# Kernel optimization log

Measured on AMD Instinct MI355X. Metric: run time of the kernel, lower is better.

## Reference

```python
import jax, jax.numpy as jnp
import numpy as np

B, NJ, COL = 16384, 14, 14
R = 4  # scipy gaussian_filter(sigma=1, truncate=4) -> radius int(4*1+0.5)=4


def _gauss_kernel(dtype):
    x = np.arange(-R, R + 1, dtype=np.float64)
    k = np.exp(-0.5 * x * x)
    k /= k.sum()
    return jnp.asarray(k, dtype)


def _gaussian_filter2d(x):
    # x: [B, Nj, COL, COL]; scipy mode='reflect' == jnp.pad mode='symmetric'
    k = _gauss_kernel(x.dtype)
    xp = jnp.pad(x, ((0, 0), (0, 0), (R, R), (R, R)), mode='symmetric')
    n = x.shape[0] * x.shape[1]
    xp = xp.reshape(n, 1, COL + 2 * R, COL + 2 * R)
    y = jax.lax.conv_general_dilated(xp, k.reshape(1, 1, 2 * R + 1, 1), (1, 1), 'VALID')
    y = jax.lax.conv_general_dilated(y, k.reshape(1, 1, 1, 2 * R + 1), (1, 1), 'VALID')
    return y.reshape(x.shape)


def setup_inputs() -> dict:
    key = jax.random.key(0)
    k1, k2, k3, k4, k5 = jax.random.split(key, 5)
    h = jax.random.uniform(k1, (B, NJ, COL, COL), jnp.float32)
    os_ = jax.random.normal(k2, (B, 2 * NJ, COL, COL), jnp.float32)
    op = jax.random.uniform(k3, (B, NJ, 3), jnp.float32)
    t = jax.random.uniform(k4, (B, NJ, 2), jnp.float32)
    vis = jax.random.randint(k5, (B, NJ, 1), 0, 2).astype(jnp.float32)
    v = jnp.concatenate([vis, vis], axis=-1)  # visibility duplicated, as assumed by v.sum()/2
    return {"os_": os_, "h": h, "op": op, "t": t, "v": v}


def reference(os_, h, op, t, v):
    scale = 1.0 / COL
    grid = jnp.arange(COL)

    # --- argmax decode of predicted heatmaps ---
    hf = h.reshape(-1, NJ, COL * COL)
    idx = jnp.argmax(hf, axis=-1)                 # [B, Nj]
    yC = idx // COL                               # integer division (old-torch LongTensor /)
    xC = idx - yC * COL
    hmax = jnp.max(hf, axis=-1)                   # h value at argmax
    osf = os_.reshape(-1, 2 * NJ, COL * COL)
    osx = jnp.take_along_axis(osf[:, :NJ], idx[..., None], axis=-1)[..., 0]
    osy = jnp.take_along_axis(osf[:, NJ:], idx[..., None], axis=-1)[..., 0]
    cond = hmax > 0.5
    x0 = jnp.where(cond, (osx + xC.astype(h.dtype)) * scale, 0.0)
    x1 = jnp.where(cond, (osy + yC.astype(h.dtype)) * scale, 0.0)
    x = jnp.stack([x0, x1], axis=-1)              # [B, Nj, 2]

    # --- gaussian splat of target coords into tt (only for visible joints) ---
    ti = t * COL
    xi = jnp.clip(jnp.trunc(ti[..., 0]).astype(jnp.int32), 0, COL - 1)
    yi = jnp.clip(jnp.trunc(ti[..., 1]).astype(jnp.int32), 0, COL - 1)
    onehot = ((grid[None, None, :, None] == yi[..., None, None]) &
              (grid[None, None, None, :] == xi[..., None, None])).astype(h.dtype)
    g = _gaussian_filter2d(onehot)
    mn = g.min(axis=(-2, -1), keepdims=True)
    mx = g.max(axis=(-2, -1), keepdims=True)
    gn = (g - mn) / (mx - mn)                     # min_max normalization
    vis = jnp.trunc(v[..., 0]).astype(jnp.int32) == 1  # int(v[i,j,0]) == 1
    tt = jnp.where(vis[..., None, None], gn, 0.0)

    # --- d1: heatmap MSE; for invisible joints only ROW 0 of diff is zeroed (faithful to source) ---
    diff1 = h - tt
    row0_mask = (~vis)[..., None, None] & (grid == 0)[None, None, :, None]
    diff1 = jnp.where(row0_mask, 0.0, diff1)
    N = v.sum() / 2
    d1 = jnp.sum(diff1 * diff1) / N

    # --- d2: decoded-coordinate MSE, visibility-masked ---
    diff2 = (x - t) * v
    d2 = jnp.sum(diff2 * diff2) / N

    return d1 + d2
```

## Files before the change

### kernel.cpp

```cpp
#include <hip/hip_runtime.h>
#include <math.h>

#define NB     16384
#define NJOINT 14
#define NCOL   14
#define NPIX   196
#define NTASKS (NB * NJOINT)
#define RAD    4

#define BLOCK1 256
#define GRID1  (NTASKS / BLOCK1)

typedef float f4 __attribute__((ext_vector_type(4)));

__global__ __launch_bounds__(BLOCK1) void mse2_main(
    const float* __restrict__ osp,
    const float* __restrict__ h,
    const float* __restrict__ t,
    const float* __restrict__ v,
    double* __restrict__ partials)
{
    __shared__ float tbl[NPIX];
    __shared__ float rmax[NCOL];
    __shared__ double sd[BLOCK1], sn[BLOCK1];

    const int tid = threadIdx.x;

    if (tid < NPIX) {
        double kd[2 * RAD + 1];
        double ks = 0.0;
        #pragma unroll
        for (int d = 0; d <= 2 * RAD; ++d) {
            double xx = (double)(d - RAD);
            kd[d] = exp(-0.5 * xx * xx);
            ks += kd[d];
        }
        const int p = tid / NCOL, o = tid % NCOL;
        float s = 0.f;
        #pragma unroll
        for (int d = 0; d <= 2 * RAD; ++d) {
            int i = o + d;
            int m = (i < RAD) ? (RAD - 1 - i)
                  : (i < RAD + NCOL) ? (i - RAD)
                  : (2 * (RAD + NCOL) - 1 - i - RAD);
            if (m == p) s += (float)(kd[d] / ks);
        }
        tbl[p * NCOL + o] = s;
    }
    __syncthreads();
    if (tid < NCOL) {
        float mxv = tbl[tid * NCOL];
        for (int o = 1; o < NCOL; ++o) mxv = fmaxf(mxv, tbl[tid * NCOL + o]);
        rmax[tid] = mxv;
    }
    __syncthreads();

    const int task = blockIdx.x * BLOCK1 + tid;

    const float2 tv = reinterpret_cast<const float2*>(t)[task];
    const float t0 = tv.x;
    const float t1 = tv.y;
    const float v0 = reinterpret_cast<const float2*>(v)[task].x;
    const bool vis = ((int)v0) == 1;
    const float visf = vis ? 1.f : 0.f;

    const int xi = min(NCOL - 1, max(0, (int)(t0 * (float)NCOL)));
    const int yi = min(NCOL - 1, max(0, (int)(t1 * (float)NCOL)));
    const float inv = 1.f / (rmax[yi] * rmax[xi]);

    float gys[NCOL], gxs[NCOL];
    #pragma unroll
    for (int k = 0; k < NCOL; ++k) {
        gys[k] = tbl[yi * NCOL + k];
        gxs[k] = vis ? tbl[xi * NCOL + k] * inv : 0.f;
    }

    const f4* __restrict__ hb4 =
        reinterpret_cast<const f4*>(h + (size_t)task * NPIX);

    float acc  = 0.f;
    float mval = -1.f;
    int   midx = 0;

    #pragma unroll
    for (int q = 0; q < NPIX / 4; ++q) {
        const f4 hv4 = hb4[q];
        #pragma unroll
        for (int j = 0; j < 4; ++j) {
            const int el = 4 * q + j;
            const int y = el / NCOL;
            const int x = el - y * NCOL;
            const float hv = hv4[j];
            if (hv > mval) { mval = hv; midx = el; }
            const float tgt = gys[y] * gxs[x];
            const float d   = hv - tgt;
            const float c   = d * d;
            acc += (y == 0) ? visf * c : c;
        }
    }

    float d2v = 0.f, nv = 0.f;
    if (vis) {
        nv = v0;
        const int yC = midx / NCOL;
        const int xC = midx - yC * NCOL;
        const int b  = task / NJOINT;
        const int j  = task - b * NJOINT;
        const float* __restrict__ ob = osp + ((size_t)b * (2 * NJOINT) + j) * NPIX;
        const float osx = ob[midx];
        const float osy = ob[(size_t)NJOINT * NPIX + midx];
        const bool cond = mval > 0.5f;
        const float sc = 1.0f / (float)NCOL;
        const float x0 = cond ? (osx + (float)xC) * sc : 0.f;
        const float x1 = cond ? (osy + (float)yC) * sc : 0.f;
        const float dx = x0 - t0;
        const float dy = x1 - t1;
        d2v = dx * dx + dy * dy;
    }

    sd[tid] = (double)acc + (double)d2v;
    sn[tid] = (double)nv;
    __syncthreads();
    #pragma unroll
    for (int off = BLOCK1 / 2; off > 0; off >>= 1) {
        if (tid < off) {
            sd[tid] += sd[tid + off];
            sn[tid] += sn[tid + off];
        }
        __syncthreads();
    }
    if (tid == 0) {
        partials[blockIdx.x * 2 + 0] = sd[0];
        partials[blockIdx.x * 2 + 1] = sn[0];
    }
}

__global__ __launch_bounds__(256) void mse2_reduce(const double* __restrict__ partials,
                                                   float* __restrict__ out)
{
    __shared__ double ssum[256], snum[256];
    double s = 0.0, n = 0.0;
    for (int i = threadIdx.x; i < GRID1; i += 256) {
        s += partials[i * 2 + 0];
        n += partials[i * 2 + 1];
    }
    ssum[threadIdx.x] = s;
    snum[threadIdx.x] = n;
    __syncthreads();
    for (int off = 128; off; off >>= 1) {
        if (threadIdx.x < off) {
            ssum[threadIdx.x] += ssum[threadIdx.x + off];
            snum[threadIdx.x] += snum[threadIdx.x + off];
        }
        __syncthreads();
    }
    if (threadIdx.x == 0) out[0] = (float)(ssum[0] / snum[0]);
}

extern "C" void kernel_launch(void* const* d_in, const int* in_sizes, int n_in,
                              void* d_out, int out_size, void* d_ws, size_t ws_size,
                              hipStream_t stream) {
    const float* osp = (const float*)d_in[0];
    const float* h   = (const float*)d_in[1];
    const float* t   = (const float*)d_in[3];
    const float* v   = (const float*)d_in[4];
    double* partials = (double*)d_ws;
    float* out = (float*)d_out;

    mse2_main<<<GRID1, BLOCK1, 0, stream>>>(osp, h, t, v, partials);
    mse2_reduce<<<1, 256, 0, stream>>>(partials, out);
}
```

Measured before the change: 42.70 us.

## Fuse final reduction into main kernel via atomics and last-block completion

```diff
diff --git a/kernel.cpp b/kernel.cpp
--- a/kernel.cpp
+++ b/kernel.cpp
@@ -13,18 +13,28 @@
 
 typedef float f4 __attribute__((ext_vector_type(4)));
 
-__global__ __launch_bounds__(BLOCK1) void mse2_main(
+
+__global__ __launch_bounds__(BLOCK1) void mse2_fused(
     const float* __restrict__ osp,
     const float* __restrict__ h,
     const float* __restrict__ t,
     const float* __restrict__ v,
-    double* __restrict__ partials)
+    double* __restrict__ acc_s,
+    double* __restrict__ acc_n,
+    unsigned int* __restrict__ counter,
+    float* __restrict__ out)
 {
     __shared__ float tbl[NPIX];
     __shared__ float rmax[NCOL];
     __shared__ double sd[BLOCK1], sn[BLOCK1];
 
     const int tid = threadIdx.x;
+
+    const int task = blockIdx.x * BLOCK1 + tid;
+    const float2 tv = reinterpret_cast<const float2*>(t)[task];
+    const float t0 = tv.x;
+    const float t1 = tv.y;
+    const float v0 = reinterpret_cast<const float2*>(v)[task].x;
 
     if (tid < NPIX) {
         double kd[2 * RAD + 1];
@@ -55,12 +65,6 @@
     }
     __syncthreads();
 
-    const int task = blockIdx.x * BLOCK1 + tid;
-
-    const float2 tv = reinterpret_cast<const float2*>(t)[task];
-    const float t0 = tv.x;
-    const float t1 = tv.y;
-    const float v0 = reinterpret_cast<const float2*>(v)[task].x;
     const bool vis = ((int)v0) == 1;
     const float visf = vis ? 1.f : 0.f;
 
@@ -129,32 +133,20 @@
         }
         __syncthreads();
     }
+
     if (tid == 0) {
-        partials[blockIdx.x * 2 + 0] = sd[0];
-        partials[blockIdx.x * 2 + 1] = sn[0];
+        atomicAdd(acc_s, sd[0]);
+        atomicAdd(acc_n, sn[0]);
+        asm volatile("s_waitcnt vmcnt(0)" ::: "memory");
+        const unsigned int old =
+            __hip_atomic_fetch_add(counter, 1u, __ATOMIC_RELAXED,
+                                   __HIP_MEMORY_SCOPE_AGENT);
+        if (old == GRID1 - 1) {
+            const double s = atomicAdd(acc_s, 0.0);
+            const double n = atomicAdd(acc_n, 0.0);
+            out[0] = (float)(s / n);
+        }
     }
-}
-
-__global__ __launch_bounds__(256) void mse2_reduce(const double* __restrict__ partials,
-                                                   float* __restrict__ out)
-{
-    __shared__ double ssum[256], snum[256];
-    double s = 0.0, n = 0.0;
-    for (int i = threadIdx.x; i < GRID1; i += 256) {
-        s += partials[i * 2 + 0];
-        n += partials[i * 2 + 1];
-    }
-    ssum[threadIdx.x] = s;
-    snum[threadIdx.x] = n;
-    __syncthreads();
-    for (int off = 128; off; off >>= 1) {
-        if (threadIdx.x < off) {
-            ssum[threadIdx.x] += ssum[threadIdx.x + off];
-            snum[threadIdx.x] += snum[threadIdx.x + off];
-        }
-        __syncthreads();
-    }
-    if (threadIdx.x == 0) out[0] = (float)(ssum[0] / snum[0]);
 }
 
 extern "C" void kernel_launch(void* const* d_in, const int* in_sizes, int n_in,
@@ -164,9 +156,12 @@
     const float* h   = (const float*)d_in[1];
     const float* t   = (const float*)d_in[3];
     const float* v   = (const float*)d_in[4];
-    double* partials = (double*)d_ws;
+
+    double* acc_s = (double*)d_ws;
+    double* acc_n = (double*)((char*)d_ws + 8);
+    unsigned int* counter = (unsigned int*)((char*)d_ws + 16);
     float* out = (float*)d_out;
 
-    mse2_main<<<GRID1, BLOCK1, 0, stream>>>(osp, h, t, v, partials);
-    mse2_reduce<<<1, 256, 0, stream>>>(partials, out);
+    hipMemsetAsync(d_ws, 0, 32, stream);
+    mse2_fused<<<GRID1, BLOCK1, 0, stream>>>(osp, h, t, v, acc_s, acc_n, counter, out);
 }
```

Result: slower. 61.69 us (+44.5%).

## Stage heatmaps through LDS with coalesced loads and split each task across four threads

Applied to the files above, without the earlier changes.

```diff
diff --git a/kernel.cpp b/kernel.cpp
--- a/kernel.cpp
+++ b/kernel.cpp
@@ -1,19 +1,21 @@
 #include <hip/hip_runtime.h>
-#include <math.h>
 
 #define NB     16384
-#define NJOINT 14
+#define NJ     14
 #define NCOL   14
 #define NPIX   196
-#define NTASKS (NB * NJOINT)
-#define RAD    4
-
-#define BLOCK1 256
-#define GRID1  (NTASKS / BLOCK1)
+#define NTASKS (NB * NJ)
+#define BLOCK  128
+#define TPG    32
+#define NGRP   4
+#define TPB    (TPG * NGRP)
+#define NBLK   (NTASKS / TPB)
+#define ST4    51
+#define GF4    (TPG * 49)
 
 typedef float f4 __attribute__((ext_vector_type(4)));
 
-__global__ __launch_bounds__(BLOCK1) void mse2_main(
+__global__ __launch_bounds__(BLOCK) void mse2_main(
     const float* __restrict__ osp,
     const float* __restrict__ h,
     const float* __restrict__ t,
@@ -22,116 +24,155 @@
 {
     __shared__ float tbl[NPIX];
     __shared__ float rmax[NCOL];
-    __shared__ double sd[BLOCK1], sn[BLOCK1];
+    __shared__ float gxst[TPG * NCOL];
+    __shared__ float hbuf[TPG * ST4 * 4];
+    __shared__ double sred[4];
 
     const int tid = threadIdx.x;
-
-    if (tid < NPIX) {
-        double kd[2 * RAD + 1];
+    const int blk = blockIdx.x;
+
+    {
+        const double KDA[5] = {1.0, 0.6065306597126334, 0.1353352832366127,
+                               0.011108996538242306, 0.00033546262790251185};
+        double kd[9];
         double ks = 0.0;
         #pragma unroll
-        for (int d = 0; d <= 2 * RAD; ++d) {
-            double xx = (double)(d - RAD);
-            kd[d] = exp(-0.5 * xx * xx);
-            ks += kd[d];
-        }
-        const int p = tid / NCOL, o = tid % NCOL;
-        float s = 0.f;
-        #pragma unroll
-        for (int d = 0; d <= 2 * RAD; ++d) {
-            int i = o + d;
-            int m = (i < RAD) ? (RAD - 1 - i)
-                  : (i < RAD + NCOL) ? (i - RAD)
-                  : (2 * (RAD + NCOL) - 1 - i - RAD);
-            if (m == p) s += (float)(kd[d] / ks);
-        }
-        tbl[p * NCOL + o] = s;
+        for (int d = 0; d < 9; ++d) { kd[d] = KDA[d < 4 ? 4 - d : d - 4]; ks += kd[d]; }
+        for (int e = tid; e < NPIX; e += BLOCK) {
+            const int p = e / NCOL, o = e % NCOL;
+            float s = 0.f;
+            #pragma unroll
+            for (int d = 0; d < 9; ++d) {
+                const int i = o + d;
+                const int m = (i < 4) ? (3 - i)
+                            : (i < 18) ? (i - 4)
+                            : (31 - i);
+                if (m == p) s += (float)(kd[d] / ks);
+            }
+            tbl[e] = s;
+        }
     }
     __syncthreads();
     if (tid < NCOL) {
-        float mxv = tbl[tid * NCOL];
-        for (int o = 1; o < NCOL; ++o) mxv = fmaxf(mxv, tbl[tid * NCOL + o]);
-        rmax[tid] = mxv;
-    }
+        float mx = tbl[tid * NCOL];
+        for (int o = 1; o < NCOL; ++o) mx = fmaxf(mx, tbl[tid * NCOL + o]);
+        rmax[tid] = mx;
+    }
+
+    const int tl = tid >> 2;
+    const int s  = tid & 3;
+    const int x0 = (7 * s) % 14;
+    const int y0 = (49 * s) / 14;
+
+    double pd = 0.0, pn = 0.0;
+    float st_mval[NGRP]; int st_midx[NGRP];
+    float st_t0[NGRP], st_t1[NGRP]; int st_vis[NGRP];
+
+    const f4* __restrict__ h4 = reinterpret_cast<const f4*>(h);
+    f4* __restrict__ hbuf4 = reinterpret_cast<f4*>(hbuf);
+
+    #pragma unroll
+    for (int g = 0; g < NGRP; ++g) {
+        const int tbase = blk * TPB + g * TPG;
+        __syncthreads();
+
+        const size_t gbase = (size_t)tbase * 49;
+        #pragma unroll
+        for (int i = 0; i < 13; ++i) {
+            const int j = tid + BLOCK * i;
+            if (j < GF4) {
+                const f4 val = h4[gbase + j];
+                const int tk = j / 49;
+                const int e  = j - tk * 49;
+                hbuf4[tk * ST4 + e] = val;
+            }
+        }
+
+        const int task = tbase + tl;
+        const float2 tv = reinterpret_cast<const float2*>(t)[task];
+        const float v0 = reinterpret_cast<const float2*>(v)[task].x;
+        const bool vis = ((int)v0) == 1;
+        const int xi = min(13, max(0, (int)(tv.x * 14.f)));
+        const int yi = min(13, max(0, (int)(tv.y * 14.f)));
+        if (s == 0) {
+            const float inv = 1.f / (rmax[yi] * rmax[xi]);
+            #pragma unroll
+            for (int o = 0; o < NCOL; ++o)
+                gxst[tl * NCOL + o] = vis ? tbl[xi * NCOL + o] * inv : 0.f;
+        }
+        __syncthreads();
+
+        const float* __restrict__ hseg = hbuf + tl * (ST4 * 4) + s * 49;
+        const float* __restrict__ gx   = gxst + tl * NCOL;
+        int x = x0, y = y0;
+        float gy = tbl[yi * NCOL + y];
+        float mval = -1.f; int midx = 0;
+        float acc = 0.f;
+        const bool zmask = (s == 0) && !vis;
+
+        #pragma unroll
+        for (int c = 0; c < 49; ++c) {
+            const float hv = hseg[c];
+            const int el = s * 49 + c;
+            if (hv > mval) { mval = hv; midx = el; }
+            const float d = hv - gy * gx[x];
+            float cc = d * d;
+            if (c < 14) { if (zmask) cc = 0.f; }
+            acc += cc;
+            ++x;
+            if (x == NCOL) { x = 0; ++y; if (c < 48) gy = tbl[yi * NCOL + y]; }
+        }
+
+        #pragma unroll
+        for (int off = 1; off <= 2; off <<= 1) {
+            const float ov = __shfl_xor(mval, off);
+            const int   oi = __shfl_xor(midx, off);
+            const float oa = __shfl_xor(acc, off);
+            acc += oa;
+            if (ov > mval || (ov == mval && oi < midx)) { mval = ov; midx = oi; }
+        }
+        if (s == 0) {
+            pd += (double)acc;
+            if (vis) pn += (double)v0;
+        }
+        st_mval[g] = mval; st_midx[g] = midx;
+        st_t0[g] = tv.x;  st_t1[g] = tv.y; st_vis[g] = vis ? 1 : 0;
+    }
+
+    if (s == 0) {
+        #pragma unroll
+        for (int g = 0; g < NGRP; ++g) {
+            if (st_vis[g]) {
+                const int task = blk * TPB + g * TPG + tl;
+                const int midx = st_midx[g];
+                const int yC = midx / NCOL;
+                const int xC = midx - yC * NCOL;
+                const int b  = task / NJ;
+                const int j  = task - b * NJ;
+                const float* __restrict__ ob = osp + ((size_t)b * (2 * NJ) + j) * NPIX;
+                const float osx = ob[midx];
+                const float osy = ob[(size_t)NJ * NPIX + midx];
+                const bool cond = st_mval[g] > 0.5f;
+                const float sc = 1.0f / 14.f;
+                const float xx0 = cond ? (osx + (float)xC) * sc : 0.f;
+                const float xx1 = cond ? (osy + (float)yC) * sc : 0.f;
+                const float dx = xx0 - st_t0[g];
+                const float dy = xx1 - st_t1[g];
+                pd += (double)(dx * dx + dy * dy);
+            }
+        }
+    }
+
+    #pragma unroll
+    for (int off = 1; off < 64; off <<= 1) {
+        pd += __shfl_xor(pd, off);
+        pn += __shfl_xor(pn, off);
+    }
+    if ((tid & 63) == 0) { sred[(tid >> 6) * 2] = pd; sred[(tid >> 6) * 2 + 1] = pn; }
     __syncthreads();
-
-    const int task = blockIdx.x * BLOCK1 + tid;
-
-    const float2 tv = reinterpret_cast<const float2*>(t)[task];
-    const float t0 = tv.x;
-    const float t1 = tv.y;
-    const float v0 = reinterpret_cast<const float2*>(v)[task].x;
-    const bool vis = ((int)v0) == 1;
-    const float visf = vis ? 1.f : 0.f;
-
-    const int xi = min(NCOL - 1, max(0, (int)(t0 * (float)NCOL)));
-    const int yi = min(NCOL - 1, max(0, (int)(t1 * (float)NCOL)));
-    const float inv = 1.f / (rmax[yi] * rmax[xi]);
-
-    float gys[NCOL], gxs[NCOL];
-    #pragma unroll
-    for (int k = 0; k < NCOL; ++k) {
-        gys[k] = tbl[yi * NCOL + k];
-        gxs[k] = vis ? tbl[xi * NCOL + k] * inv : 0.f;
-    }
-
-    const f4* __restrict__ hb4 =
-        reinterpret_cast<const f4*>(h + (size_t)task * NPIX);
-
-    float acc  = 0.f;
-    float mval = -1.f;
-    int   midx = 0;
-
-    #pragma unroll
-    for (int q = 0; q < NPIX / 4; ++q) {
-        const f4 hv4 = hb4[q];
-        #pragma unroll
-        for (int j = 0; j < 4; ++j) {
-            const int el = 4 * q + j;
-            const int y = el / NCOL;
-            const int x = el - y * NCOL;
-            const float hv = hv4[j];
-            if (hv > mval) { mval = hv; midx = el; }
-            const float tgt = gys[y] * gxs[x];
-            const float d   = hv - tgt;
-            const float c   = d * d;
-            acc += (y == 0) ? visf * c : c;
-        }
-    }
-
-    float d2v = 0.f, nv = 0.f;
-    if (vis) {
-        nv = v0;
-        const int yC = midx / NCOL;
-        const int xC = midx - yC * NCOL;
-        const int b  = task / NJOINT;
-        const int j  = task - b * NJOINT;
-        const float* __restrict__ ob = osp + ((size_t)b * (2 * NJOINT) + j) * NPIX;
-        const float osx = ob[midx];
-        const float osy = ob[(size_t)NJOINT * NPIX + midx];
-        const bool cond = mval > 0.5f;
-        const float sc = 1.0f / (float)NCOL;
-        const float x0 = cond ? (osx + (float)xC) * sc : 0.f;
-        const float x1 = cond ? (osy + (float)yC) * sc : 0.f;
-        const float dx = x0 - t0;
-        const float dy = x1 - t1;
-        d2v = dx * dx + dy * dy;
-    }
-
-    sd[tid] = (double)acc + (double)d2v;
-    sn[tid] = (double)nv;
-    __syncthreads();
-    #pragma unroll
-    for (int off = BLOCK1 / 2; off > 0; off >>= 1) {
-        if (tid < off) {
-            sd[tid] += sd[tid + off];
-            sn[tid] += sn[tid + off];
-        }
-        __syncthreads();
-    }
     if (tid == 0) {
-        partials[blockIdx.x * 2 + 0] = sd[0];
-        partials[blockIdx.x * 2 + 1] = sn[0];
+        partials[blk * 2 + 0] = sred[0] + sred[2];
+        partials[blk * 2 + 1] = sred[1] + sred[3];
     }
 }
 
@@ -139,12 +180,12 @@
                                                    float* __restrict__ out)
 {
     __shared__ double ssum[256], snum[256];
-    double s = 0.0, n = 0.0;
-    for (int i = threadIdx.x; i < GRID1; i += 256) {
-        s += partials[i * 2 + 0];
-        n += partials[i * 2 + 1];
-    }
-    ssum[threadIdx.x] = s;
+    double sv = 0.0, n = 0.0;
+    for (int i = threadIdx.x; i < NBLK; i += 256) {
+        sv += partials[i * 2 + 0];
+        n  += partials[i * 2 + 1];
+    }
+    ssum[threadIdx.x] = sv;
     snum[threadIdx.x] = n;
     __syncthreads();
     for (int off = 128; off; off >>= 1) {
@@ -167,6 +208,6 @@
     double* partials = (double*)d_ws;
     float* out = (float*)d_out;
 
-    mse2_main<<<GRID1, BLOCK1, 0, stream>>>(osp, h, t, v, partials);
+    mse2_main<<<NBLK, BLOCK, 0, stream>>>(osp, h, t, v, partials);
     mse2_reduce<<<1, 256, 0, stream>>>(partials, out);
 }
```

New measurement: 69.33 us. +62.4%, slower.
